# Kernel tuning notes

Hardware: AMD Instinct MI355X
Metric: run time of the kernel (lower is better)

Reference implementation:

```python
import jax, jax.numpy as jnp
import numpy as np

N = 50000      # nodes
E = 800000     # edges
F = 128        # node_features
EF = 16        # edge_features
H = 128        # hidden_features
OUT = 128      # out_features
L = 4          # num_layers
G = 16         # graphs in batch


def setup_inputs() -> dict:
    key = jax.random.key(0)
    ks = jax.random.split(key, 24)
    s = 0.05
    w = lambda k, shape: (jax.random.normal(k, shape, jnp.float32) * s)
    inp = {
        "x": jax.random.normal(ks[0], (N, F), jnp.float32),
        "edge_index": jax.random.randint(ks[1], (2, E), 0, N, jnp.int64),
        "edge_attr": jax.random.normal(ks[2], (E, EF), jnp.float32),
        "batch": jnp.sort(jax.random.randint(ks[3], (N,), 0, G, jnp.int64)),
        # embedder
        "embW": w(ks[4], (F, H)), "embb": jnp.zeros((H,), jnp.float32),
        # per-layer message net: Linear(2H+EF->H), ReLU, Linear(H->H), ReLU
        "msgW1": w(ks[5], (L, 2 * H + EF, H)), "msgb1": jnp.zeros((L, H), jnp.float32),
        "msgW2": w(ks[6], (L, H, H)), "msgb2": jnp.zeros((L, H), jnp.float32),
        # per-layer update net: Linear(H+H->H), ReLU, Linear(H->H)
        "updW1": w(ks[7], (L, 2 * H, H)), "updb1": jnp.zeros((L, H), jnp.float32),
        "updW2": w(ks[8], (L, H, H)), "updb2": jnp.zeros((L, H), jnp.float32),
        # pre/post pool MLPs
        "preW1": w(ks[9], (H, H)), "preb1": jnp.zeros((H,), jnp.float32),
        "preW2": w(ks[10], (H, H)), "preb2": jnp.zeros((H,), jnp.float32),
        "postW1": w(ks[11], (H, H)), "postb1": jnp.zeros((H,), jnp.float32),
        "postW2": w(ks[12], (H, OUT)), "postb2": jnp.zeros((OUT,), jnp.float32),
    }
    return inp


def reference(x, edge_index, edge_attr, batch,
              embW, embb,
              msgW1, msgb1, msgW2, msgb2,
              updW1, updb1, updW2, updb2,
              preW1, preb1, preW2, preb2,
              postW1, postb1, postW2, postb2):
    src = edge_index[0]  # j (source)
    dst = edge_index[1]  # i (target, aggregation index)
    h = x @ embW + embb  # [N, H]
    for l in range(L):
        # message: cat(x_i, x_j, edge_attr) -> MLP -> ReLU
        m = jnp.concatenate([h[dst], h[src], edge_attr], axis=-1)  # [E, 2H+EF]
        m = jax.nn.relu(m @ msgW1[l] + msgb1[l])
        m = jax.nn.relu(m @ msgW2[l] + msgb2[l])
        # aggregate 'add' at target nodes
        agg = jax.ops.segment_sum(m, dst, num_segments=N)  # [N, H]
        # update: cat(x, message) -> MLP
        u = jnp.concatenate([h, agg], axis=-1)  # [N, 2H]
        u = jax.nn.relu(u @ updW1[l] + updb1[l])
        u = u @ updW2[l] + updb2[l]
        h = h + u  # residual (x += layer(x, ...))
    # pre_pool MLP
    p = jax.nn.relu(h @ preW1 + preb1) @ preW2 + preb2  # [N, H]
    # global add pool per graph
    g = jax.ops.segment_sum(p, batch, num_segments=G)  # [G, H]
    # post_pool MLP
    out = jax.nn.relu(g @ postW1 + postb1) @ postW2 + postb2  # [G, OUT]
    return out
```

## Files before the change

kernel.cpp:

```cpp
#include <hip/hip_runtime.h>

typedef __attribute__((ext_vector_type(8))) short bf16x8;
typedef __attribute__((ext_vector_type(8))) unsigned short u16x8;
typedef __attribute__((ext_vector_type(4))) float f32x4;
typedef unsigned short u16;
typedef unsigned int u32;

#define NN 50000
#define NE 800000

static __device__ __forceinline__ u16 f2bf(float f) {
  u32 u = __builtin_bit_cast(u32, f);
  u = (u + 0x7fffu + ((u >> 16) & 1u)) >> 16;
  return (u16)u;
}
static __device__ __forceinline__ float relu_f(float v) { return v > 0.f ? v : 0.f; }

__global__ void k_hist(const int* __restrict__ dstI, int* __restrict__ counts) {
  int e = blockIdx.x * 256 + threadIdx.x;
  if (e < NE) atomicAdd(&counts[dstI[e]], 1);
}

__global__ __launch_bounds__(1024) void k_scan(const int* __restrict__ counts, int* __restrict__ cur) {
  __shared__ int part[1024];
  int t = threadIdx.x;
  const int CH = (NN + 1023) / 1024;
  int base = t * CH;
  int s = 0;
  for (int i = 0; i < CH; ++i) {
    int idx = base + i;
    s += (idx < NN) ? counts[idx] : 0;
  }
  part[t] = s;
  __syncthreads();
  for (int off = 1; off < 1024; off <<= 1) {
    int v = (t >= off) ? part[t - off] : 0;
    __syncthreads();
    part[t] += v;
    __syncthreads();
  }
  int pre = (t == 0) ? 0 : part[t - 1];
  for (int i = 0; i < CH; ++i) {
    int idx = base + i;
    if (idx < NN) {
      cur[idx] = pre;
      pre += counts[idx];
    }
  }
}

__global__ void k_scatter(const int* __restrict__ dstI, int* __restrict__ cur, int* __restrict__ eperm) {
  int e = blockIdx.x * 256 + threadIdx.x;
  if (e < NE) {
    int d = dstI[e];
    int pos = atomicAdd(&cur[d], 1);
    eperm[pos] = e;
  }
}

__global__ void k_permute(const int* __restrict__ eperm,
                          const int* __restrict__ srcI, const int* __restrict__ dstI,
                          const float* __restrict__ ea,
                          int* __restrict__ srcS, int* __restrict__ dstS, u16* __restrict__ eaS) {
  int i = blockIdx.x * 256 + threadIdx.x;
  if (i >= NE) return;
  int e = eperm[i];
  srcS[i] = srcI[e];
  dstS[i] = dstI[e];
  const float4* ev = (const float4*)(ea + (size_t)e * 16);
  float4 a = ev[0], b = ev[1], c = ev[2], d = ev[3];
  u16x8 o0, o1;
  o0[0] = f2bf(a.x); o0[1] = f2bf(a.y); o0[2] = f2bf(a.z); o0[3] = f2bf(a.w);
  o0[4] = f2bf(b.x); o0[5] = f2bf(b.y); o0[6] = f2bf(b.z); o0[7] = f2bf(b.w);
  o1[0] = f2bf(c.x); o1[1] = f2bf(c.y); o1[2] = f2bf(c.z); o1[3] = f2bf(c.w);
  o1[4] = f2bf(d.x); o1[5] = f2bf(d.y); o1[6] = f2bf(d.z); o1[7] = f2bf(d.w);
  *(u16x8*)(eaS + (size_t)i * 16) = o0;
  *(u16x8*)(eaS + (size_t)i * 16 + 8) = o1;
}

struct PackArgs {
  const float* src[19];
  u16* dst[19];
  int K[19];
  int Kpad[19];
};

__global__ void k_pack_all(PackArgs a) {
  int di = blockIdx.x / 144;
  int idx = (blockIdx.x - di * 144) * 256 + threadIdx.x;
  int Kpad = a.Kpad[di];
  if (idx >= 128 * Kpad) return;
  int c = idx / Kpad;
  int k = idx - c * Kpad;
  a.dst[di][idx] = (k < a.K[di]) ? f2bf(a.src[di][(size_t)k * 128 + c]) : (u16)0;
}

__global__ __launch_bounds__(256, 2) void k_embed(
    const float* __restrict__ x, const u16* __restrict__ WT, const float* __restrict__ bias,
    float* __restrict__ h, u16* __restrict__ h_bf)
{
  __shared__ __align__(16) u16 A1[64][136];
  const int t = threadIdx.x;
  const int wv = t >> 6, ln = t & 63;
  const int l15 = ln & 15, hi = ln >> 4;
  const int col0 = wv * 32;

  bf16x8 wf[4][2];
#pragma unroll
  for (int kb = 0; kb < 4; ++kb)
#pragma unroll
    for (int nb = 0; nb < 2; ++nb)
      wf[kb][nb] = *(const bf16x8*)(WT + (col0 + nb * 16 + l15) * 128 + kb * 32 + hi * 8);
  float bv[2];
#pragma unroll
  for (int nb = 0; nb < 2; ++nb) bv[nb] = bias[col0 + nb * 16 + l15];

  const int r = t >> 2, p = t & 3;
  const int tile = blockIdx.x;
  {
    int node = tile * 64 + r;
    if (node < NN) {
      const float4* xv = (const float4*)(x + (size_t)node * 128) + p * 8;
#pragma unroll
      for (int i = 0; i < 4; ++i) {
        float4 v0 = xv[2 * i], v1 = xv[2 * i + 1];
        u16x8 o;
        o[0] = f2bf(v0.x); o[1] = f2bf(v0.y); o[2] = f2bf(v0.z); o[3] = f2bf(v0.w);
        o[4] = f2bf(v1.x); o[5] = f2bf(v1.y); o[6] = f2bf(v1.z); o[7] = f2bf(v1.w);
        *(u16x8*)(&A1[r][p * 32 + i * 8]) = o;
      }
    }
  }
  __syncthreads();

  f32x4 acc[4][2];
#pragma unroll
  for (int rb = 0; rb < 4; ++rb)
#pragma unroll
    for (int nb = 0; nb < 2; ++nb) acc[rb][nb] = (f32x4){0.f, 0.f, 0.f, 0.f};
#pragma unroll
  for (int kb = 0; kb < 4; ++kb) {
    bf16x8 af[4];
#pragma unroll
    for (int rb = 0; rb < 4; ++rb)
      af[rb] = *(const bf16x8*)(&A1[rb * 16 + l15][kb * 32 + hi * 8]);
#pragma unroll
    for (int rb = 0; rb < 4; ++rb)
#pragma unroll
      for (int nb = 0; nb < 2; ++nb)
        acc[rb][nb] = __builtin_amdgcn_mfma_f32_16x16x32_bf16(af[rb], wf[kb][nb], acc[rb][nb], 0, 0, 0);
  }
#pragma unroll
  for (int rb = 0; rb < 4; ++rb)
#pragma unroll
    for (int nb = 0; nb < 2; ++nb)
#pragma unroll
      for (int i = 0; i < 4; ++i) {
        int row = rb * 16 + hi * 4 + i;
        int node = tile * 64 + row;
        if (node < NN) {
          int col = col0 + nb * 16 + l15;
          float v = acc[rb][nb][i] + bv[nb];
          size_t ix = (size_t)node * 128 + col;
          h[ix] = v;
          h_bf[ix] = f2bf(v);
        }
      }
}

__global__ __launch_bounds__(256, 4) void k_edge(
    const int* __restrict__ srcS, const int* __restrict__ dstS,
    const u16* __restrict__ h_bf, const u16* __restrict__ eaS,
    const u16* __restrict__ W1T, const float* __restrict__ b1,
    const u16* __restrict__ W2T, const float* __restrict__ b2,
    float* __restrict__ agg)
{
  __shared__ __align__(16) u16 SH[64 * 296];
  __shared__ int dstL[64];
  float* SHf = (float*)SH;

  const int t = threadIdx.x;
  const int wv = t >> 6, ln = t & 63;
  const int l15 = ln & 15, hi = ln >> 4;
  const int col0 = wv * 32;

  bf16x8 w1f[9][2], w2f[4][2];
#pragma unroll
  for (int kb = 0; kb < 9; ++kb)
#pragma unroll
    for (int nb = 0; nb < 2; ++nb)
      w1f[kb][nb] = *(const bf16x8*)(W1T + (col0 + nb * 16 + l15) * 288 + kb * 32 + hi * 8);
#pragma unroll
  for (int kb = 0; kb < 4; ++kb)
#pragma unroll
    for (int nb = 0; nb < 2; ++nb)
      w2f[kb][nb] = *(const bf16x8*)(W2T + (col0 + nb * 16 + l15) * 128 + kb * 32 + hi * 8);
  float b1v[2], b2v[2];
#pragma unroll
  for (int nb = 0; nb < 2; ++nb) {
    b1v[nb] = b1[col0 + nb * 16 + l15];
    b2v[nb] = b2[col0 + nb * 16 + l15];
  }

  const int r = t >> 2, p = t & 3;
  const int NT = NE / 64;

  int tile = blockIdx.x;
  int s_nx = srcS[tile * 64 + r];
  int d_nx = dstS[tile * 64 + r];

  for (; tile < NT; tile += gridDim.x) {
    {
      int e = tile * 64 + r;
      int s = s_nx, d = d_nx;
      if (p == 0) dstL[r] = d;
      const uint4* hd = (const uint4*)(h_bf + (size_t)d * 128) + p * 4;
      const uint4* hs = (const uint4*)(h_bf + (size_t)s * 128) + p * 4;
      uint4* a0 = (uint4*)(&SH[r * 296]) + p * 4;
      uint4* a1 = (uint4*)(&SH[r * 296 + 128]) + p * 4;
#pragma unroll
      for (int i = 0; i < 4; ++i) { a0[i] = hd[i]; a1[i] = hs[i]; }
      if (p == 1) {
        const uint4* ea = (const uint4*)(eaS + (size_t)e * 16);
        uint4* aE = (uint4*)(&SH[r * 296 + 256]);
        aE[0] = ea[0]; aE[1] = ea[1];
      } else if (p == 2) {
        uint4 z = make_uint4(0, 0, 0, 0);
        uint4* aZ = (uint4*)(&SH[r * 296 + 272]);
        aZ[0] = z;
      }
      int tn = tile + gridDim.x;
      if (tn < NT) {
        int en = tn * 64 + r;
        s_nx = srcS[en];
        d_nx = dstS[en];
      }
    }
    __syncthreads();

    f32x4 acc1[4][2];
#pragma unroll
    for (int rb = 0; rb < 4; ++rb)
#pragma unroll
      for (int nb = 0; nb < 2; ++nb) acc1[rb][nb] = (f32x4){0.f, 0.f, 0.f, 0.f};
#pragma unroll
    for (int kb = 0; kb < 9; ++kb) {
      bf16x8 af[4];
#pragma unroll
      for (int rb = 0; rb < 4; ++rb)
        af[rb] = *(const bf16x8*)(&SH[(rb * 16 + l15) * 296 + kb * 32 + hi * 8]);
#pragma unroll
      for (int rb = 0; rb < 4; ++rb)
#pragma unroll
        for (int nb = 0; nb < 2; ++nb)
          acc1[rb][nb] = __builtin_amdgcn_mfma_f32_16x16x32_bf16(af[rb], w1f[kb][nb], acc1[rb][nb], 0, 0, 0);
    }
    __syncthreads();

#pragma unroll
    for (int rb = 0; rb < 4; ++rb)
#pragma unroll
      for (int nb = 0; nb < 2; ++nb)
#pragma unroll
        for (int i = 0; i < 4; ++i) {
          float v = acc1[rb][nb][i] + b1v[nb];
          SH[(rb * 16 + hi * 4 + i) * 136 + col0 + nb * 16 + l15] = f2bf(relu_f(v));
        }
    __syncthreads();

    f32x4 acc2[4][2];
#pragma unroll
    for (int rb = 0; rb < 4; ++rb)
#pragma unroll
      for (int nb = 0; nb < 2; ++nb) acc2[rb][nb] = (f32x4){0.f, 0.f, 0.f, 0.f};
#pragma unroll
    for (int kb = 0; kb < 4; ++kb) {
      bf16x8 af[4];
#pragma unroll
      for (int rb = 0; rb < 4; ++rb)
        af[rb] = *(const bf16x8*)(&SH[(rb * 16 + l15) * 136 + kb * 32 + hi * 8]);
#pragma unroll
      for (int rb = 0; rb < 4; ++rb)
#pragma unroll
        for (int nb = 0; nb < 2; ++nb)
          acc2[rb][nb] = __builtin_amdgcn_mfma_f32_16x16x32_bf16(af[rb], w2f[kb][nb], acc2[rb][nb], 0, 0, 0);
    }
    __syncthreads();

#pragma unroll
    for (int rb = 0; rb < 4; ++rb)
#pragma unroll
      for (int nb = 0; nb < 2; ++nb)
#pragma unroll
        for (int i = 0; i < 4; ++i) {
          float v = relu_f(acc2[rb][nb][i] + b2v[nb]);
          SHf[(rb * 16 + hi * 4 + i) * 132 + col0 + nb * 16 + l15] = v;
        }
    __syncthreads();

    {
      int c = t & 127, hh = t >> 7;
      int r0 = hh * 32;
      int d0 = dstL[r0];
      float run = SHf[r0 * 132 + c];
#pragma unroll 4
      for (int rr = r0 + 1; rr < r0 + 32; ++rr) {
        int d = dstL[rr];
        float v = SHf[rr * 132 + c];
        if (d != d0) {
          atomicAdd(&agg[(size_t)d0 * 128 + c], run);
          d0 = d; run = v;
        } else {
          run += v;
        }
      }
      atomicAdd(&agg[(size_t)d0 * 128 + c], run);
    }
    __syncthreads();
  }
}

__global__ __launch_bounds__(256, 4) void k_node_update(
    const float* __restrict__ aggIn,
    const u16* __restrict__ W1T, const float* __restrict__ b1,
    const u16* __restrict__ W2T, const float* __restrict__ b2,
    float* __restrict__ h, u16* __restrict__ h_bf)
{
  __shared__ __align__(16) u16 SH[64 * 264];
  const int t = threadIdx.x;
  const int wv = t >> 6, ln = t & 63;
  const int l15 = ln & 15, hi = ln >> 4;
  const int col0 = wv * 32;

  bf16x8 w1f[8][2], w2f[4][2];
#pragma unroll
  for (int kb = 0; kb < 8; ++kb)
#pragma unroll
    for (int nb = 0; nb < 2; ++nb)
      w1f[kb][nb] = *(const bf16x8*)(W1T + (col0 + nb * 16 + l15) * 256 + kb * 32 + hi * 8);
#pragma unroll
  for (int kb = 0; kb < 4; ++kb)
#pragma unroll
    for (int nb = 0; nb < 2; ++nb)
      w2f[kb][nb] = *(const bf16x8*)(W2T + (col0 + nb * 16 + l15) * 128 + kb * 32 + hi * 8);
  float b1v[2], b2v[2];
#pragma unroll
  for (int nb = 0; nb < 2; ++nb) {
    b1v[nb] = b1[col0 + nb * 16 + l15];
    b2v[nb] = b2[col0 + nb * 16 + l15];
  }

  const int r = t >> 2, p = t & 3;
  const int tile = blockIdx.x;
  {
    int node = tile * 64 + r;
    if (node < NN) {
      const uint4* hv = (const uint4*)(h_bf + (size_t)node * 128) + p * 4;
      uint4* a0 = (uint4*)(&SH[r * 264]) + p * 4;
#pragma unroll
      for (int i = 0; i < 4; ++i) a0[i] = hv[i];
      const float4* ag = (const float4*)(aggIn + (size_t)node * 128) + p * 8;
#pragma unroll
      for (int i = 0; i < 4; ++i) {
        float4 v0 = ag[2 * i], v1 = ag[2 * i + 1];
        u16x8 o;
        o[0] = f2bf(v0.x); o[1] = f2bf(v0.y); o[2] = f2bf(v0.z); o[3] = f2bf(v0.w);
        o[4] = f2bf(v1.x); o[5] = f2bf(v1.y); o[6] = f2bf(v1.z); o[7] = f2bf(v1.w);
        *(u16x8*)(&SH[r * 264 + 128 + p * 32 + i * 8]) = o;
      }
    }
  }
  __syncthreads();

  f32x4 acc1[4][2];
#pragma unroll
  for (int rb = 0; rb < 4; ++rb)
#pragma unroll
    for (int nb = 0; nb < 2; ++nb) acc1[rb][nb] = (f32x4){0.f, 0.f, 0.f, 0.f};
#pragma unroll
  for (int kb = 0; kb < 8; ++kb) {
    bf16x8 af[4];
#pragma unroll
    for (int rb = 0; rb < 4; ++rb)
      af[rb] = *(const bf16x8*)(&SH[(rb * 16 + l15) * 264 + kb * 32 + hi * 8]);
#pragma unroll
    for (int rb = 0; rb < 4; ++rb)
#pragma unroll
      for (int nb = 0; nb < 2; ++nb)
        acc1[rb][nb] = __builtin_amdgcn_mfma_f32_16x16x32_bf16(af[rb], w1f[kb][nb], acc1[rb][nb], 0, 0, 0);
  }
  __syncthreads();

#pragma unroll
  for (int rb = 0; rb < 4; ++rb)
#pragma unroll
    for (int nb = 0; nb < 2; ++nb)
#pragma unroll
      for (int i = 0; i < 4; ++i) {
        float v = acc1[rb][nb][i] + b1v[nb];
        SH[(rb * 16 + hi * 4 + i) * 136 + col0 + nb * 16 + l15] = f2bf(relu_f(v));
      }
  __syncthreads();

  f32x4 acc2[4][2];
#pragma unroll
  for (int rb = 0; rb < 4; ++rb)
#pragma unroll
    for (int nb = 0; nb < 2; ++nb) acc2[rb][nb] = (f32x4){0.f, 0.f, 0.f, 0.f};
#pragma unroll
  for (int kb = 0; kb < 4; ++kb) {
    bf16x8 af[4];
#pragma unroll
    for (int rb = 0; rb < 4; ++rb)
      af[rb] = *(const bf16x8*)(&SH[(rb * 16 + l15) * 136 + kb * 32 + hi * 8]);
#pragma unroll
    for (int rb = 0; rb < 4; ++rb)
#pragma unroll
      for (int nb = 0; nb < 2; ++nb)
        acc2[rb][nb] = __builtin_amdgcn_mfma_f32_16x16x32_bf16(af[rb], w2f[kb][nb], acc2[rb][nb], 0, 0, 0);
  }
#pragma unroll
  for (int rb = 0; rb < 4; ++rb)
#pragma unroll
    for (int nb = 0; nb < 2; ++nb)
#pragma unroll
      for (int i = 0; i < 4; ++i) {
        int row = rb * 16 + hi * 4 + i;
        int node = tile * 64 + row;
        if (node < NN) {
          int col = col0 + nb * 16 + l15;
          float v = acc2[rb][nb][i] + b2v[nb];
          size_t ix = (size_t)node * 128 + col;
          float nh = h[ix] + v;
          h[ix] = nh;
          h_bf[ix] = f2bf(nh);
        }
      }
}

__global__ __launch_bounds__(256, 4) void k_prepool(
    const u16* __restrict__ h_bf, const int* __restrict__ batch,
    const u16* __restrict__ W1T, const float* __restrict__ b1,
    const u16* __restrict__ W2T, const float* __restrict__ b2,
    float* __restrict__ g)
{
  __shared__ __align__(16) u16 SH[64 * 272];
  __shared__ int bL[64];
  float* SHf = (float*)SH;
  const int t = threadIdx.x;
  const int wv = t >> 6, ln = t & 63;
  const int l15 = ln & 15, hi = ln >> 4;
  const int col0 = wv * 32;

  bf16x8 w1f[4][2], w2f[4][2];
#pragma unroll
  for (int kb = 0; kb < 4; ++kb)
#pragma unroll
    for (int nb = 0; nb < 2; ++nb) {
      w1f[kb][nb] = *(const bf16x8*)(W1T + (col0 + nb * 16 + l15) * 128 + kb * 32 + hi * 8);
      w2f[kb][nb] = *(const bf16x8*)(W2T + (col0 + nb * 16 + l15) * 128 + kb * 32 + hi * 8);
    }
  float b1v[2], b2v[2];
#pragma unroll
  for (int nb = 0; nb < 2; ++nb) {
    b1v[nb] = b1[col0 + nb * 16 + l15];
    b2v[nb] = b2[col0 + nb * 16 + l15];
  }

  const int r = t >> 2, p = t & 3;
  const int tile = blockIdx.x;
  {
    int node = tile * 64 + r;
    int nclamp = node < NN ? node : NN - 1;
    if (p == 0) bL[r] = batch[nclamp];
    if (node < NN) {
      const uint4* hv = (const uint4*)(h_bf + (size_t)node * 128) + p * 4;
      uint4* a0 = (uint4*)(&SH[r * 136]) + p * 4;
#pragma unroll
      for (int i = 0; i < 4; ++i) a0[i] = hv[i];
    }
  }
  __syncthreads();

  f32x4 acc1[4][2];
#pragma unroll
  for (int rb = 0; rb < 4; ++rb)
#pragma unroll
    for (int nb = 0; nb < 2; ++nb) acc1[rb][nb] = (f32x4){0.f, 0.f, 0.f, 0.f};
#pragma unroll
  for (int kb = 0; kb < 4; ++kb) {
    bf16x8 af[4];
#pragma unroll
    for (int rb = 0; rb < 4; ++rb)
      af[rb] = *(const bf16x8*)(&SH[(rb * 16 + l15) * 136 + kb * 32 + hi * 8]);
#pragma unroll
    for (int rb = 0; rb < 4; ++rb)
#pragma unroll
      for (int nb = 0; nb < 2; ++nb)
        acc1[rb][nb] = __builtin_amdgcn_mfma_f32_16x16x32_bf16(af[rb], w1f[kb][nb], acc1[rb][nb], 0, 0, 0);
  }
#pragma unroll
  for (int rb = 0; rb < 4; ++rb)
#pragma unroll
    for (int nb = 0; nb < 2; ++nb)
#pragma unroll
      for (int i = 0; i < 4; ++i) {
        float v = acc1[rb][nb][i] + b1v[nb];
        SH[64 * 136 + (rb * 16 + hi * 4 + i) * 136 + col0 + nb * 16 + l15] = f2bf(relu_f(v));
      }
  __syncthreads();

  f32x4 acc2[4][2];
#pragma unroll
  for (int rb = 0; rb < 4; ++rb)
#pragma unroll
    for (int nb = 0; nb < 2; ++nb) acc2[rb][nb] = (f32x4){0.f, 0.f, 0.f, 0.f};
#pragma unroll
  for (int kb = 0; kb < 4; ++kb) {
    bf16x8 af[4];
#pragma unroll
    for (int rb = 0; rb < 4; ++rb)
      af[rb] = *(const bf16x8*)(&SH[64 * 136 + (rb * 16 + l15) * 136 + kb * 32 + hi * 8]);
#pragma unroll
    for (int rb = 0; rb < 4; ++rb)
#pragma unroll
      for (int nb = 0; nb < 2; ++nb)
        acc2[rb][nb] = __builtin_amdgcn_mfma_f32_16x16x32_bf16(af[rb], w2f[kb][nb], acc2[rb][nb], 0, 0, 0);
  }
  __syncthreads();

#pragma unroll
  for (int rb = 0; rb < 4; ++rb)
#pragma unroll
    for (int nb = 0; nb < 2; ++nb)
#pragma unroll
      for (int i = 0; i < 4; ++i) {
        int row = rb * 16 + hi * 4 + i;
        int node = tile * 64 + row;
        float v = acc2[rb][nb][i] + b2v[nb];
        SHf[row * 132 + col0 + nb * 16 + l15] = (node < NN) ? v : 0.f;
      }
  __syncthreads();

  {
    int c = t & 127, hh = t >> 7;
    int r0 = hh * 32;
    int b0 = bL[r0];
    float run = SHf[r0 * 132 + c];
#pragma unroll 4
    for (int rr = r0 + 1; rr < r0 + 32; ++rr) {
      int b = bL[rr];
      float v = SHf[rr * 132 + c];
      if (b != b0) {
        atomicAdd(&g[(size_t)b0 * 128 + c], run);
        b0 = b; run = v;
      } else {
        run += v;
      }
    }
    atomicAdd(&g[(size_t)b0 * 128 + c], run);
  }
}

__global__ void k_postpool(const float* __restrict__ g,
                           const float* __restrict__ W1, const float* __restrict__ b1,
                           const float* __restrict__ W2, const float* __restrict__ b2,
                           float* __restrict__ out)
{
  __shared__ float gl[16][128];
  __shared__ float t1[16][129];
  int t = threadIdx.x;
  for (int i = t; i < 16 * 128; i += 256) gl[i >> 7][i & 127] = g[i];
  __syncthreads();
  for (int o = t; o < 16 * 128; o += 256) {
    int r = o >> 7, c = o & 127;
    float s = b1[c];
    for (int k = 0; k < 128; ++k) s += gl[r][k] * W1[k * 128 + c];
    t1[r][c] = relu_f(s);
  }
  __syncthreads();
  for (int o = t; o < 16 * 128; o += 256) {
    int r = o >> 7, c = o & 127;
    float s = b2[c];
    for (int k = 0; k < 128; ++k) s += t1[r][k] * W2[k * 128 + c];
    out[o] = s;
  }
}

extern "C" void kernel_launch(void* const* d_in, const int* in_sizes, int n_in,
                              void* d_out, int out_size, void* d_ws, size_t ws_size,
                              hipStream_t stream) {
  (void)in_sizes; (void)n_in; (void)out_size; (void)ws_size;
  const float* x      = (const float*)d_in[0];
  const int*   ei     = (const int*)d_in[1];
  const float* ea     = (const float*)d_in[2];
  const int*   batch  = (const int*)d_in[3];
  const float* embW   = (const float*)d_in[4];
  const float* embb   = (const float*)d_in[5];
  const float* msgW1  = (const float*)d_in[6];
  const float* msgb1  = (const float*)d_in[7];
  const float* msgW2  = (const float*)d_in[8];
  const float* msgb2  = (const float*)d_in[9];
  const float* updW1  = (const float*)d_in[10];
  const float* updb1  = (const float*)d_in[11];
  const float* updW2  = (const float*)d_in[12];
  const float* updb2  = (const float*)d_in[13];
  const float* preW1  = (const float*)d_in[14];
  const float* preb1  = (const float*)d_in[15];
  const float* preW2  = (const float*)d_in[16];
  const float* preb2  = (const float*)d_in[17];
  const float* postW1 = (const float*)d_in[18];
  const float* postb1 = (const float*)d_in[19];
  const float* postW2 = (const float*)d_in[20];
  const float* postb2 = (const float*)d_in[21];

  const int* srcI = ei;
  const int* dstI = ei + NE;

  char* ws = (char*)d_ws;
  size_t off = 0;
  auto alloc = [&](size_t bytes) -> void* {
    void* pp = ws + off;
    off += (bytes + 255) & ~(size_t)255;
    return pp;
  };
  float* h      = (float*)alloc((size_t)NN * 128 * 4);
  float* agg    = (float*)alloc((size_t)NN * 128 * 4);
  float* g      = (float*)alloc(16 * 128 * 4);
  u16*   h_bf   = (u16*)alloc((size_t)NN * 128 * 2);
  u16*   eaS    = (u16*)alloc((size_t)NE * 16 * 2);
  int*   counts = (int*)alloc((size_t)NN * 4);
  int*   cur    = (int*)alloc((size_t)NN * 4);
  int*   eperm  = (int*)alloc((size_t)NE * 4);
  int*   srcS   = (int*)alloc((size_t)NE * 4);
  int*   dstS   = (int*)alloc((size_t)NE * 4);
  u16*   embWT  = (u16*)alloc(128 * 128 * 2);
  u16*   msgW1T = (u16*)alloc(4 * 128 * 288 * 2);
  u16*   msgW2T = (u16*)alloc(4 * 128 * 128 * 2);
  u16*   updW1T = (u16*)alloc(4 * 128 * 256 * 2);
  u16*   updW2T = (u16*)alloc(4 * 128 * 128 * 2);
  u16*   preW1T = (u16*)alloc(128 * 128 * 2);
  u16*   preW2T = (u16*)alloc(128 * 128 * 2);

  hipMemsetAsync(counts, 0, (size_t)NN * 4, stream);
  const int eBlocks = (NE + 255) / 256;
  k_hist<<<eBlocks, 256, 0, stream>>>(dstI, counts);
  k_scan<<<1, 1024, 0, stream>>>(counts, cur);
  k_scatter<<<eBlocks, 256, 0, stream>>>(dstI, cur, eperm);
  k_permute<<<eBlocks, 256, 0, stream>>>(eperm, srcI, dstI, ea, srcS, dstS, eaS);

  {
    PackArgs pa;
    int di = 0;
    auto add = [&](const float* s, u16* dp, int K, int Kpad) {
      pa.src[di] = s; pa.dst[di] = dp; pa.K[di] = K; pa.Kpad[di] = Kpad; ++di;
    };
    add(embW, embWT, 128, 128);
    for (int l = 0; l < 4; ++l) add(msgW1 + (size_t)l * 272 * 128, msgW1T + (size_t)l * 128 * 288, 272, 288);
    for (int l = 0; l < 4; ++l) add(msgW2 + (size_t)l * 128 * 128, msgW2T + (size_t)l * 128 * 128, 128, 128);
    for (int l = 0; l < 4; ++l) add(updW1 + (size_t)l * 256 * 128, updW1T + (size_t)l * 128 * 256, 256, 256);
    for (int l = 0; l < 4; ++l) add(updW2 + (size_t)l * 128 * 128, updW2T + (size_t)l * 128 * 128, 128, 128);
    add(preW1, preW1T, 128, 128);
    add(preW2, preW2T, 128, 128);
    k_pack_all<<<19 * 144, 256, 0, stream>>>(pa);
  }

  const int nodeTiles = (NN + 63) / 64;
  k_embed<<<nodeTiles, 256, 0, stream>>>(x, embWT, embb, h, h_bf);

  for (int l = 0; l < 4; ++l) {
    hipMemsetAsync(agg, 0, (size_t)NN * 128 * 4, stream);
    k_edge<<<1024, 256, 0, stream>>>(srcS, dstS, h_bf, eaS,
                                     msgW1T + (size_t)l * 128 * 288, msgb1 + l * 128,
                                     msgW2T + (size_t)l * 128 * 128, msgb2 + l * 128, agg);
    k_node_update<<<nodeTiles, 256, 0, stream>>>(agg,
                                    updW1T + (size_t)l * 128 * 256, updb1 + l * 128,
                                    updW2T + (size_t)l * 128 * 128, updb2 + l * 128,
                                    h, h_bf);
  }

  hipMemsetAsync(g, 0, 16 * 128 * 4, stream);
  k_prepool<<<nodeTiles, 256, 0, stream>>>(h_bf, batch, preW1T, preb1, preW2T, preb2, g);
  k_postpool<<<1, 256, 0, stream>>>(g, postW1, postb1, postW2, postb2, (float*)d_out);
}
```

Before: 1.233 ms.

## Use 8 waves per edge block, each owning 16 output columns

The edge message kernel moves from 4 waves of 256 threads, each computing 32 output columns, to 8 waves of 512 threads, each computing 16 columns. This halves the per-thread weight fragments and accumulators, which cuts register pressure and allows more waves in flight to hide gather latency. The gather is spread over 8 threads per row instead of 4. The segmented atomic reduction still uses only the first 256 threads, and more waves now wait at each barrier.

```diff
diff --git a/kernel.cpp b/kernel.cpp
--- a/kernel.cpp
+++ b/kernel.cpp
@@ -168,7 +168,7 @@
       }
 }
 
-__global__ __launch_bounds__(256, 4) void k_edge(
+__global__ __launch_bounds__(512, 8) void k_edge(
     const int* __restrict__ srcS, const int* __restrict__ dstS,
     const u16* __restrict__ h_bf, const u16* __restrict__ eaS,
     const u16* __restrict__ W1T, const float* __restrict__ b1,
@@ -182,27 +182,19 @@
   const int t = threadIdx.x;
   const int wv = t >> 6, ln = t & 63;
   const int l15 = ln & 15, hi = ln >> 4;
-  const int col0 = wv * 32;
-
-  bf16x8 w1f[9][2], w2f[4][2];
+  const int col0 = wv * 16;
+
+  bf16x8 w1f[9], w2f[4];
 #pragma unroll
   for (int kb = 0; kb < 9; ++kb)
-#pragma unroll
-    for (int nb = 0; nb < 2; ++nb)
-      w1f[kb][nb] = *(const bf16x8*)(W1T + (col0 + nb * 16 + l15) * 288 + kb * 32 + hi * 8);
+    w1f[kb] = *(const bf16x8*)(W1T + (col0 + l15) * 288 + kb * 32 + hi * 8);
 #pragma unroll
   for (int kb = 0; kb < 4; ++kb)
-#pragma unroll
-    for (int nb = 0; nb < 2; ++nb)
-      w2f[kb][nb] = *(const bf16x8*)(W2T + (col0 + nb * 16 + l15) * 128 + kb * 32 + hi * 8);
-  float b1v[2], b2v[2];
-#pragma unroll
-  for (int nb = 0; nb < 2; ++nb) {
-    b1v[nb] = b1[col0 + nb * 16 + l15];
-    b2v[nb] = b2[col0 + nb * 16 + l15];
-  }
-
-  const int r = t >> 2, p = t & 3;
+    w2f[kb] = *(const bf16x8*)(W2T + (col0 + l15) * 128 + kb * 32 + hi * 8);
+  const float b1v = b1[col0 + l15];
+  const float b2v = b2[col0 + l15];
+
+  const int r = t >> 3, p = t & 7;
   const int NT = NE / 64;
 
   int tile = blockIdx.x;
@@ -214,20 +206,20 @@
       int e = tile * 64 + r;
       int s = s_nx, d = d_nx;
       if (p == 0) dstL[r] = d;
-      const uint4* hd = (const uint4*)(h_bf + (size_t)d * 128) + p * 4;
-      const uint4* hs = (const uint4*)(h_bf + (size_t)s * 128) + p * 4;
-      uint4* a0 = (uint4*)(&SH[r * 296]) + p * 4;
-      uint4* a1 = (uint4*)(&SH[r * 296 + 128]) + p * 4;
-#pragma unroll
-      for (int i = 0; i < 4; ++i) { a0[i] = hd[i]; a1[i] = hs[i]; }
-      if (p == 1) {
+      const uint4* hd = (const uint4*)(h_bf + (size_t)d * 128) + p * 2;
+      const uint4* hs = (const uint4*)(h_bf + (size_t)s * 128) + p * 2;
+      uint4* a0 = (uint4*)(&SH[r * 296]) + p * 2;
+      uint4* a1 = (uint4*)(&SH[r * 296 + 128]) + p * 2;
+      a0[0] = hd[0]; a0[1] = hd[1];
+      a1[0] = hs[0]; a1[1] = hs[1];
+      if (p == 4) {
         const uint4* ea = (const uint4*)(eaS + (size_t)e * 16);
         uint4* aE = (uint4*)(&SH[r * 296 + 256]);
         aE[0] = ea[0]; aE[1] = ea[1];
-      } else if (p == 2) {
+      } else if (p == 5) {
         uint4 z = make_uint4(0, 0, 0, 0);
         uint4* aZ = (uint4*)(&SH[r * 296 + 272]);
-        aZ[0] = z;
+        aZ[0] = z; aZ[1] = z;
       }
       int tn = tile + gridDim.x;
       if (tn < NT) {
@@ -238,11 +230,9 @@
     }
     __syncthreads();
 
-    f32x4 acc1[4][2];
-#pragma unroll
-    for (int rb = 0; rb < 4; ++rb)
-#pragma unroll
-      for (int nb = 0; nb < 2; ++nb) acc1[rb][nb] = (f32x4){0.f, 0.f, 0.f, 0.f};
+    f32x4 acc1[4];
+#pragma unroll
+    for (int rb = 0; rb < 4; ++rb) acc1[rb] = (f32x4){0.f, 0.f, 0.f, 0.f};
 #pragma unroll
     for (int kb = 0; kb < 9; ++kb) {
       bf16x8 af[4];
@@ -251,28 +241,22 @@
         af[rb] = *(const bf16x8*)(&SH[(rb * 16 + l15) * 296 + kb * 32 + hi * 8]);
 #pragma unroll
       for (int rb = 0; rb < 4; ++rb)
-#pragma unroll
-        for (int nb = 0; nb < 2; ++nb)
-          acc1[rb][nb] = __builtin_amdgcn_mfma_f32_16x16x32_bf16(af[rb], w1f[kb][nb], acc1[rb][nb], 0, 0, 0);
-    }
-    __syncthreads();
-
-#pragma unroll
-    for (int rb = 0; rb < 4; ++rb)
-#pragma unroll
-      for (int nb = 0; nb < 2; ++nb)
-#pragma unroll
-        for (int i = 0; i < 4; ++i) {
-          float v = acc1[rb][nb][i] + b1v[nb];
-          SH[(rb * 16 + hi * 4 + i) * 136 + col0 + nb * 16 + l15] = f2bf(relu_f(v));
-        }
-    __syncthreads();
-
-    f32x4 acc2[4][2];
-#pragma unroll
-    for (int rb = 0; rb < 4; ++rb)
-#pragma unroll
-      for (int nb = 0; nb < 2; ++nb) acc2[rb][nb] = (f32x4){0.f, 0.f, 0.f, 0.f};
+        acc1[rb] = __builtin_amdgcn_mfma_f32_16x16x32_bf16(af[rb], w1f[kb], acc1[rb], 0, 0, 0);
+    }
+    __syncthreads();
+
+#pragma unroll
+    for (int rb = 0; rb < 4; ++rb)
+#pragma unroll
+      for (int i = 0; i < 4; ++i) {
+        float v = acc1[rb][i] + b1v;
+        SH[(rb * 16 + hi * 4 + i) * 136 + col0 + l15] = f2bf(relu_f(v));
+      }
+    __syncthreads();
+
+    f32x4 acc2[4];
+#pragma unroll
+    for (int rb = 0; rb < 4; ++rb) acc2[rb] = (f32x4){0.f, 0.f, 0.f, 0.f};
 #pragma unroll
     for (int kb = 0; kb < 4; ++kb) {
       bf16x8 af[4];
@@ -281,24 +265,20 @@
         af[rb] = *(const bf16x8*)(&SH[(rb * 16 + l15) * 136 + kb * 32 + hi * 8]);
 #pragma unroll
       for (int rb = 0; rb < 4; ++rb)
-#pragma unroll
-        for (int nb = 0; nb < 2; ++nb)
-          acc2[rb][nb] = __builtin_amdgcn_mfma_f32_16x16x32_bf16(af[rb], w2f[kb][nb], acc2[rb][nb], 0, 0, 0);
-    }
-    __syncthreads();
-
-#pragma unroll
-    for (int rb = 0; rb < 4; ++rb)
-#pragma unroll
-      for (int nb = 0; nb < 2; ++nb)
-#pragma unroll
-        for (int i = 0; i < 4; ++i) {
-          float v = relu_f(acc2[rb][nb][i] + b2v[nb]);
-          SHf[(rb * 16 + hi * 4 + i) * 132 + col0 + nb * 16 + l15] = v;
-        }
-    __syncthreads();
-
-    {
+        acc2[rb] = __builtin_amdgcn_mfma_f32_16x16x32_bf16(af[rb], w2f[kb], acc2[rb], 0, 0, 0);
+    }
+    __syncthreads();
+
+#pragma unroll
+    for (int rb = 0; rb < 4; ++rb)
+#pragma unroll
+      for (int i = 0; i < 4; ++i) {
+        float v = relu_f(acc2[rb][i] + b2v);
+        SHf[(rb * 16 + hi * 4 + i) * 132 + col0 + l15] = v;
+      }
+    __syncthreads();
+
+    if (t < 256) {
       int c = t & 127, hh = t >> 7;
       int r0 = hh * 32;
       int d0 = dstL[r0];
@@ -670,7 +650,7 @@
 
   for (int l = 0; l < 4; ++l) {
     hipMemsetAsync(agg, 0, (size_t)NN * 128 * 4, stream);
-    k_edge<<<1024, 256, 0, stream>>>(srcS, dstS, h_bf, eaS,
+    k_edge<<<1024, 512, 0, stream>>>(srcS, dstS, h_bf, eaS,
                                      msgW1T + (size_t)l * 128 * 288, msgb1 + l * 128,
                                      msgW2T + (size_t)l * 128 * 128, msgb2 + l * 128, agg);
     k_node_update<<<nodeTiles, 256, 0, stream>>>(agg,
```

New measurement: 1.385 ms. +12.3%, slower.

## Precompute per-node dst projection of message W1 and gather it per edge

Applied to the files above, without the earlier changes.

Splits the first message linear layer so the h[dst] part is computed once per node in a new k_qdst kernel, producing an fp32 Q buffer. The edge kernel then initialises its accumulators from Q[dst] and runs only the source-plus-edge-attribute part, cutting K from 288 to 160. Edges are sorted by dst, so Q rows are reused across neighbouring edges. In exchange it adds a per-layer node GEMM, a 25.6MB fp32 buffer and scattered fp32 gathers in the edge loop. It also changes precision slightly, since the dst contribution is now kept in fp32 rather than bf16 MFMA inputs.

```diff
diff --git a/kernel.cpp b/kernel.cpp
--- a/kernel.cpp
+++ b/kernel.cpp
@@ -79,10 +79,10 @@
 }
 
 struct PackArgs {
-  const float* src[19];
-  u16* dst[19];
-  int K[19];
-  int Kpad[19];
+  const float* src[24];
+  u16* dst[24];
+  int K[24];
+  int Kpad[24];
 };
 
 __global__ void k_pack_all(PackArgs a) {
@@ -168,28 +168,88 @@
       }
 }
 
-__global__ __launch_bounds__(256, 4) void k_edge(
-    const int* __restrict__ srcS, const int* __restrict__ dstS,
-    const u16* __restrict__ h_bf, const u16* __restrict__ eaS,
-    const u16* __restrict__ W1T, const float* __restrict__ b1,
-    const u16* __restrict__ W2T, const float* __restrict__ b2,
-    float* __restrict__ agg)
+__global__ __launch_bounds__(256, 2) void k_qdst(
+    const u16* __restrict__ h_bf, const u16* __restrict__ WT, float* __restrict__ Q)
 {
-  __shared__ __align__(16) u16 SH[64 * 296];
-  __shared__ int dstL[64];
-  float* SHf = (float*)SH;
-
+  __shared__ __align__(16) u16 A1[64][136];
   const int t = threadIdx.x;
   const int wv = t >> 6, ln = t & 63;
   const int l15 = ln & 15, hi = ln >> 4;
   const int col0 = wv * 32;
 
-  bf16x8 w1f[9][2], w2f[4][2];
-#pragma unroll
-  for (int kb = 0; kb < 9; ++kb)
-#pragma unroll
-    for (int nb = 0; nb < 2; ++nb)
-      w1f[kb][nb] = *(const bf16x8*)(W1T + (col0 + nb * 16 + l15) * 288 + kb * 32 + hi * 8);
+  bf16x8 wf[4][2];
+#pragma unroll
+  for (int kb = 0; kb < 4; ++kb)
+#pragma unroll
+    for (int nb = 0; nb < 2; ++nb)
+      wf[kb][nb] = *(const bf16x8*)(WT + (col0 + nb * 16 + l15) * 128 + kb * 32 + hi * 8);
+
+  const int r = t >> 2, p = t & 3;
+  const int tile = blockIdx.x;
+  {
+    int node = tile * 64 + r;
+    if (node < NN) {
+      const uint4* hv = (const uint4*)(h_bf + (size_t)node * 128) + p * 4;
+      uint4* a0 = (uint4*)(&A1[r][0]) + p * 4;
+#pragma unroll
+      for (int i = 0; i < 4; ++i) a0[i] = hv[i];
+    }
+  }
+  __syncthreads();
+
+  f32x4 acc[4][2];
+#pragma unroll
+  for (int rb = 0; rb < 4; ++rb)
+#pragma unroll
+    for (int nb = 0; nb < 2; ++nb) acc[rb][nb] = (f32x4){0.f, 0.f, 0.f, 0.f};
+#pragma unroll
+  for (int kb = 0; kb < 4; ++kb) {
+    bf16x8 af[4];
+#pragma unroll
+    for (int rb = 0; rb < 4; ++rb)
+      af[rb] = *(const bf16x8*)(&A1[rb * 16 + l15][kb * 32 + hi * 8]);
+#pragma unroll
+    for (int rb = 0; rb < 4; ++rb)
+#pragma unroll
+      for (int nb = 0; nb < 2; ++nb)
+        acc[rb][nb] = __builtin_amdgcn_mfma_f32_16x16x32_bf16(af[rb], wf[kb][nb], acc[rb][nb], 0, 0, 0);
+  }
+#pragma unroll
+  for (int rb = 0; rb < 4; ++rb)
+#pragma unroll
+    for (int nb = 0; nb < 2; ++nb)
+#pragma unroll
+      for (int i = 0; i < 4; ++i) {
+        int row = rb * 16 + hi * 4 + i;
+        int node = tile * 64 + row;
+        if (node < NN)
+          Q[(size_t)node * 128 + col0 + nb * 16 + l15] = acc[rb][nb][i];
+      }
+}
+
+__global__ __launch_bounds__(256, 4) void k_edge(
+    const int* __restrict__ srcS, const int* __restrict__ dstS,
+    const u16* __restrict__ h_bf, const u16* __restrict__ eaS,
+    const float* __restrict__ Q,
+    const u16* __restrict__ W1sT, const float* __restrict__ b1,
+    const u16* __restrict__ W2T, const float* __restrict__ b2,
+    float* __restrict__ agg)
+{
+  __shared__ __align__(16) u16 SH[64 * 264];
+  __shared__ int dstL[64];
+  float* SHf = (float*)SH;
+
+  const int t = threadIdx.x;
+  const int wv = t >> 6, ln = t & 63;
+  const int l15 = ln & 15, hi = ln >> 4;
+  const int col0 = wv * 32;
+
+  bf16x8 w1f[5][2], w2f[4][2];
+#pragma unroll
+  for (int kb = 0; kb < 5; ++kb)
+#pragma unroll
+    for (int nb = 0; nb < 2; ++nb)
+      w1f[kb][nb] = *(const bf16x8*)(W1sT + (col0 + nb * 16 + l15) * 160 + kb * 32 + hi * 8);
 #pragma unroll
   for (int kb = 0; kb < 4; ++kb)
 #pragma unroll
@@ -210,24 +270,34 @@
   int d_nx = dstS[tile * 64 + r];
 
   for (; tile < NT; tile += gridDim.x) {
+    f32x4 acc1[4][2];
     {
       int e = tile * 64 + r;
-      int s = s_nx, d = d_nx;
-      if (p == 0) dstL[r] = d;
-      const uint4* hd = (const uint4*)(h_bf + (size_t)d * 128) + p * 4;
+      int s = s_nx;
+      if (p == 0) dstL[r] = d_nx;
       const uint4* hs = (const uint4*)(h_bf + (size_t)s * 128) + p * 4;
-      uint4* a0 = (uint4*)(&SH[r * 296]) + p * 4;
-      uint4* a1 = (uint4*)(&SH[r * 296 + 128]) + p * 4;
-#pragma unroll
-      for (int i = 0; i < 4; ++i) { a0[i] = hd[i]; a1[i] = hs[i]; }
+      uint4* a1 = (uint4*)(&SH[r * 168]) + p * 4;
+#pragma unroll
+      for (int i = 0; i < 4; ++i) a1[i] = hs[i];
       if (p == 1) {
         const uint4* ea = (const uint4*)(eaS + (size_t)e * 16);
-        uint4* aE = (uint4*)(&SH[r * 296 + 256]);
+        uint4* aE = (uint4*)(&SH[r * 168 + 128]);
         aE[0] = ea[0]; aE[1] = ea[1];
       } else if (p == 2) {
         uint4 z = make_uint4(0, 0, 0, 0);
-        uint4* aZ = (uint4*)(&SH[r * 296 + 272]);
-        aZ[0] = z;
+        uint4* aZ = (uint4*)(&SH[r * 168 + 144]);
+        aZ[0] = z; aZ[1] = z;
+      }
+      int e0 = tile * 64;
+#pragma unroll
+      for (int rb = 0; rb < 4; ++rb) {
+#pragma unroll
+        for (int i = 0; i < 4; ++i) {
+          int dr = dstS[e0 + rb * 16 + hi * 4 + i];
+          const float* qp = Q + (size_t)dr * 128 + col0 + l15;
+          acc1[rb][0][i] = qp[0];
+          acc1[rb][1][i] = qp[16];
+        }
       }
       int tn = tile + gridDim.x;
       if (tn < NT) {
@@ -238,17 +308,12 @@
     }
     __syncthreads();
 
-    f32x4 acc1[4][2];
-#pragma unroll
-    for (int rb = 0; rb < 4; ++rb)
-#pragma unroll
-      for (int nb = 0; nb < 2; ++nb) acc1[rb][nb] = (f32x4){0.f, 0.f, 0.f, 0.f};
-#pragma unroll
-    for (int kb = 0; kb < 9; ++kb) {
+#pragma unroll
+    for (int kb = 0; kb < 5; ++kb) {
       bf16x8 af[4];
 #pragma unroll
       for (int rb = 0; rb < 4; ++rb)
-        af[rb] = *(const bf16x8*)(&SH[(rb * 16 + l15) * 296 + kb * 32 + hi * 8]);
+        af[rb] = *(const bf16x8*)(&SH[(rb * 16 + l15) * 168 + kb * 32 + hi * 8]);
 #pragma unroll
       for (int rb = 0; rb < 4; ++rb)
 #pragma unroll
@@ -626,6 +691,7 @@
   };
   float* h      = (float*)alloc((size_t)NN * 128 * 4);
   float* agg    = (float*)alloc((size_t)NN * 128 * 4);
+  float* Q      = (float*)alloc((size_t)NN * 128 * 4);
   float* g      = (float*)alloc(16 * 128 * 4);
   u16*   h_bf   = (u16*)alloc((size_t)NN * 128 * 2);
   u16*   eaS    = (u16*)alloc((size_t)NE * 16 * 2);
@@ -635,7 +701,8 @@
   int*   srcS   = (int*)alloc((size_t)NE * 4);
   int*   dstS   = (int*)alloc((size_t)NE * 4);
   u16*   embWT  = (u16*)alloc(128 * 128 * 2);
-  u16*   msgW1T = (u16*)alloc(4 * 128 * 288 * 2);
+  u16*   msgW1dT = (u16*)alloc(4 * 128 * 128 * 2);
+  u16*   msgW1sT = (u16*)alloc(4 * 128 * 160 * 2);
   u16*   msgW2T = (u16*)alloc(4 * 128 * 128 * 2);
   u16*   updW1T = (u16*)alloc(4 * 128 * 256 * 2);
   u16*   updW2T = (u16*)alloc(4 * 128 * 128 * 2);
@@ -656,22 +723,24 @@
       pa.src[di] = s; pa.dst[di] = dp; pa.K[di] = K; pa.Kpad[di] = Kpad; ++di;
     };
     add(embW, embWT, 128, 128);
-    for (int l = 0; l < 4; ++l) add(msgW1 + (size_t)l * 272 * 128, msgW1T + (size_t)l * 128 * 288, 272, 288);
+    for (int l = 0; l < 4; ++l) add(msgW1 + (size_t)l * 272 * 128, msgW1dT + (size_t)l * 128 * 128, 128, 128);
+    for (int l = 0; l < 4; ++l) add(msgW1 + (size_t)l * 272 * 128 + 128 * 128, msgW1sT + (size_t)l * 128 * 160, 144, 160);
     for (int l = 0; l < 4; ++l) add(msgW2 + (size_t)l * 128 * 128, msgW2T + (size_t)l * 128 * 128, 128, 128);
     for (int l = 0; l < 4; ++l) add(updW1 + (size_t)l * 256 * 128, updW1T + (size_t)l * 128 * 256, 256, 256);
     for (int l = 0; l < 4; ++l) add(updW2 + (size_t)l * 128 * 128, updW2T + (size_t)l * 128 * 128, 128, 128);
     add(preW1, preW1T, 128, 128);
     add(preW2, preW2T, 128, 128);
-    k_pack_all<<<19 * 144, 256, 0, stream>>>(pa);
+    k_pack_all<<<23 * 144, 256, 0, stream>>>(pa);
   }
 
   const int nodeTiles = (NN + 63) / 64;
   k_embed<<<nodeTiles, 256, 0, stream>>>(x, embWT, embb, h, h_bf);
 
   for (int l = 0; l < 4; ++l) {
+    k_qdst<<<nodeTiles, 256, 0, stream>>>(h_bf, msgW1dT + (size_t)l * 128 * 128, Q);
     hipMemsetAsync(agg, 0, (size_t)NN * 128 * 4, stream);
-    k_edge<<<1024, 256, 0, stream>>>(srcS, dstS, h_bf, eaS,
-                                     msgW1T + (size_t)l * 128 * 288, msgb1 + l * 128,
+    k_edge<<<1024, 256, 0, stream>>>(srcS, dstS, h_bf, eaS, Q,
+                                     msgW1sT + (size_t)l * 128 * 160, msgb1 + l * 128,
                                      msgW2T + (size_t)l * 128 * 128, msgb2 + l * 128, agg);
     k_node_update<<<nodeTiles, 256, 0, stream>>>(agg,
                                     updW1T + (size_t)l * 128 * 256, updb1 + l * 128,
```

New measurement: 1.139 ms. 7.6% less time.
